# Optimization experiments

Hardware: AMD Instinct MI355X
Metric: run time of the kernel (lower is better)

The kernel has to match this reference:

```python
import jax, jax.numpy as jnp
import numpy as np
from jax import lax

BS, CI, NI, HI, WI = 16, 32, 8, 20, 20
CO, NO = 32, 8
ITERATIONS = 3


def setup_inputs() -> dict:
    key = jax.random.key(0)
    k1, k2 = jax.random.split(key)
    x = jax.random.normal(k1, (BS, CI, NI, HI, WI), dtype=jnp.float32)
    # conv weight: out_channels = co*no = 256, in_channels = ni = 8, 3x3
    W = jax.random.normal(k2, (CO * NO, NI, 3, 3), dtype=jnp.float32) * 0.05
    bias = jnp.zeros((CO, NO, 1, 1), dtype=jnp.float32)
    return {"x": x, "W": W, "bias": bias}


def squash(s, axis):
    # v = (|s|^2 / (1+|s|^2)) * s / |s|
    n2 = jnp.sum(s * s, axis=axis, keepdims=True)
    return s * (n2 / ((1.0 + n2) * jnp.sqrt(n2 + 1e-9)))


def reference(x, W, bias):
    bs, ci, ni, hi, wi = x.shape
    xr = x.reshape(bs * ci, ni, hi, wi)
    # conv2d, stride 1, padding 1, no bias
    votes = lax.conv_general_dilated(
        xr, W, window_strides=(1, 1), padding=[(1, 1), (1, 1)],
        dimension_numbers=("NCHW", "OIHW", "NCHW"))
    ho, wo = votes.shape[-2:]
    votes = votes.reshape(bs, ci, CO, NO, ho, wo)  # (bs,ci,co,no,ho,wo)
    logits = jnp.zeros((bs, ci, CO, ho, wo), dtype=votes.dtype)
    activation = None
    for _ in range(ITERATIONS):
        route = jax.nn.softmax(logits, axis=2)               # (bs,ci,co,ho,wo)
        # weighted sum of votes over input capsules ci, plus bias
        preact = jnp.sum(route[:, :, :, None] * votes, axis=1) + bias  # (bs,co,no,ho,wo)
        activation = squash(preact, axis=2)
        # agreement: dot over output atoms no
        distances = jnp.sum(votes * activation[:, None], axis=3)  # (bs,ci,co,ho,wo)
        logits = logits + distances
    return activation
```

## Files before the change

### kernel.cpp

```cpp
#include <hip/hip_runtime.h>

#define HH 20
#define WW 20

typedef _Float16 f16x8 __attribute__((ext_vector_type(8)));
typedef float    f32x4  __attribute__((ext_vector_type(4)));
typedef float    f32x4u __attribute__((ext_vector_type(4), aligned(4)));

__global__ void prepack_w_kernel(const float* __restrict__ Wt, _Float16* __restrict__ bp) {
    int idx = blockIdx.x * 256 + threadIdx.x;
    int oc = idx / 96, k = idx % 96;
    int r = k >> 3, ni = k & 7;
    float v = (r < 9) ? Wt[oc * 72 + ni * 9 + r] : 0.f;
    bp[idx] = (_Float16)v;
}

template<int DS>
__device__ __forceinline__ void stage_seg(const float* __restrict__ x,
                                          _Float16* A,
                                          int b, int h, int w0, int t) {
#pragma unroll
    for (int s = t; s < 768; s += 256) {
        int ci = s / 24;
        int r  = s % 24;
        int ni = r / 3, hr = r % 3;
        int hh = h - 1 + hr;
        bool hok = (hh >= 0) && (hh < HH);
        const int wlo = (DS == 0) ? (w0 - 1) : (DS < 0 ? 0 : WW - 4);
        const float* rowp = x + ((((b * 32 + ci) * 8 + ni) * HH + (hok ? hh : 0)) * WW) + wlo;
        f32x4u f4 = *(const f32x4u*)rowp;
        float vals[4];
        if (DS == 0)      { vals[0] = f4.x; vals[1] = f4.y; vals[2] = f4.z; vals[3] = f4.w; }
        else if (DS < 0)  { vals[0] = 0.f;  vals[1] = f4.x; vals[2] = f4.y; vals[3] = f4.z; }
        else              { vals[0] = f4.y; vals[1] = f4.z; vals[2] = f4.w; vals[3] = 0.f; }
        int kb = hr * 24 + ni;
#pragma unroll
        for (int j = 0; j < 4; ++j) {
            float v = hok ? vals[j] : 0.f;
            _Float16 hv = (_Float16)v;
            if (j < 3)
                A[ci * 96 + kb + j * 8] = hv;
            if (j > 0)
                A[(32 + ci) * 96 + kb + (j - 1) * 8] = hv;
        }
    }
}

__global__ __launch_bounds__(256, 3)
void caps_mfma8_kernel(const float* __restrict__ x,
                       const _Float16* __restrict__ bp,
                       const float* __restrict__ bias,
                       float* __restrict__ out) {
    __shared__ __align__(16) unsigned char region[30976];
    _Float16* A    = (_Float16*)region;
    float* bufbase = (float*)(region + 12288);

    const int t  = threadIdx.x;
    const int wv = t >> 6;
    const int lr = t & 15;
    const int lg = (t >> 4) & 3;

    const int bi  = blockIdx.x;
    const int b   = bi / 200;
    const int rem = bi % 200;
    const int h   = rem / 10;
    const int w0  = (rem % 10) * 2;

#pragma unroll
    for (int e = t; e < 768; e += 256) {
        int row = e / 12, j = e % 12;
        ((unsigned int*)(A + row * 96 + 72))[j] = 0u;
    }

    const int dshift = (w0 == 0) ? -1 : (w0 == WW - 2) ? 1 : 0;
    if (dshift == 0)      stage_seg<0>(x, A, b, h, w0, t);
    else if (dshift < 0)  stage_seg<-1>(x, A, b, h, w0, t);
    else                  stage_seg<1>(x, A, b, h, w0, t);
    __syncthreads();

    f32x4 acc[4][4];
#pragma unroll
    for (int i = 0; i < 4; ++i)
#pragma unroll
        for (int mt = 0; mt < 4; ++mt) acc[i][mt] = (f32x4){0.f, 0.f, 0.f, 0.f};

#pragma unroll
    for (int mh = 0; mh < 2; ++mh) {
#pragma unroll
        for (int kst = 0; kst < 3; ++kst) {
            const int kb = kst * 32 + lg * 8;
            f16x8 a0 = *(const f16x8*)&A[(mh * 32 + lr) * 96 + kb];
            f16x8 a1 = *(const f16x8*)&A[(mh * 32 + 16 + lr) * 96 + kb];
#pragma unroll
            for (int i = 0; i < 4; ++i) {
                const int oc = (wv * 4 + i) * 16 + lr;
                f16x8 bv = *(const f16x8*)&bp[oc * 96 + kb];
                acc[i][mh*2+0] = __builtin_amdgcn_mfma_f32_16x16x32_f16(a0, bv, acc[i][mh*2+0], 0, 0, 0);
                acc[i][mh*2+1] = __builtin_amdgcn_mfma_f32_16x16x32_f16(a1, bv, acc[i][mh*2+1], 0, 0, 0);
            }
        }
    }

    float* buf = bufbase + wv * 1152;
    float vcol[2][32];
    f32x4 vr[2][4][2];
    const int ch_t = (t >> 5) & 1;
    const int colr = t & 31;
    const int c8   = t & 24;

#pragma unroll
    for (int p = 0; p < 2; ++p) {
#pragma unroll
        for (int ch = 0; ch < 2; ++ch) {
#pragma unroll
            for (int ii = 0; ii < 2; ++ii) {
#pragma unroll
                for (int mm = 0; mm < 2; ++mm) {
#pragma unroll
                    for (int r = 0; r < 4; ++r)
                        buf[(mm * 16 + lg * 4 + r) * 36 + ii * 16 + lr] =
                            acc[ch * 2 + ii][p * 2 + mm][r];
                }
            }
            if (ch_t == ch) {
#pragma unroll
                for (int ci = 0; ci < 32; ++ci) vcol[p][ci] = buf[ci * 36 + colr];
#pragma unroll
                for (int q = 0; q < 4; ++q) {
                    int ciq = (t & 7) * 4 + q;
                    vr[p][q][0] = *(const f32x4*)&buf[ciq * 36 + c8];
                    vr[p][q][1] = *(const f32x4*)&buf[ciq * 36 + c8 + 4];
                }
            }
        }
    }

    const int co = t >> 3;
    const int no = t & 7;
    const float bsv = bias[t];
    float* route0 = bufbase;
    float* route1 = bufbase + 1152;
    float (*lg0)[37] = (float (*)[37])(bufbase + 2304);
    float (*lg1)[37] = (float (*)[37])(bufbase + 2304 + 1184);
    float dlog[2][4];
    float act[2];
    const int lbase = t & 56;

#pragma unroll
    for (int px = 0; px < 2; ++px) {
        float p = 0.f;
#pragma unroll
        for (int ci = 0; ci < 32; ++ci) p += vcol[px][ci];
        p = fmaf(p, 0.03125f, bsv);
        float n2 = p * p;
        n2 += __shfl_xor(n2, 1); n2 += __shfl_xor(n2, 2); n2 += __shfl_xor(n2, 4);
        act[px] = p * n2 * __builtin_amdgcn_rcpf(1.f + n2) * __builtin_amdgcn_rsqf(n2 + 1e-9f);

        float a[8];
#pragma unroll
        for (int j = 0; j < 8; ++j) a[j] = __shfl(act[px], lbase | j);
#pragma unroll
        for (int q = 0; q < 4; ++q) {
            f32x4 v0 = vr[px][q][0], v1 = vr[px][q][1];
            dlog[px][q] = v0.x * a[0] + v0.y * a[1] + v0.z * a[2] + v0.w * a[3]
                        + v1.x * a[4] + v1.y * a[5] + v1.z * a[6] + v1.w * a[7];
        }
    }
    __syncthreads();
#pragma unroll
    for (int px = 0; px < 2; ++px) {
        float (*lgp)[37] = px ? lg1 : lg0;
#pragma unroll
        for (int q = 0; q < 4; ++q) lgp[no * 4 + q][co] = dlog[px][q];
    }
    __syncthreads();

#pragma unroll
    for (int it = 1; it < 3; ++it) {
#pragma unroll
        for (int px = 0; px < 2; ++px) {
            float (*lgp)[37] = px ? lg1 : lg0;
            float* rtp = px ? route1 : route0;
            float l0 = lgp[co][no],      l1 = lgp[co][no + 8];
            float l2 = lgp[co][no + 16], l3 = lgp[co][no + 24];
            float m = fmaxf(fmaxf(l0, l1), fmaxf(l2, l3));
            m = fmaxf(m, __shfl_xor(m, 1)); m = fmaxf(m, __shfl_xor(m, 2)); m = fmaxf(m, __shfl_xor(m, 4));
            float e0 = __expf(l0 - m), e1 = __expf(l1 - m);
            float e2 = __expf(l2 - m), e3 = __expf(l3 - m);
            float s = e0 + e1 + e2 + e3;
            s += __shfl_xor(s, 1); s += __shfl_xor(s, 2); s += __shfl_xor(s, 4);
            float inv = __builtin_amdgcn_rcpf(s);
            rtp[(no)      * 36 + co] = e0 * inv;
            rtp[(no + 8)  * 36 + co] = e1 * inv;
            rtp[(no + 16) * 36 + co] = e2 * inv;
            rtp[(no + 24) * 36 + co] = e3 * inv;
        }
        __syncthreads();

#pragma unroll
        for (int px = 0; px < 2; ++px) {
            float* rtp = px ? route1 : route0;
            float p = bsv;
#pragma unroll
            for (int j = 0; j < 8; ++j) {
                f32x4 rv = *(const f32x4*)&rtp[co * 36 + j * 4];
                p = fmaf(rv.x, vcol[px][j * 4 + 0], p);
                p = fmaf(rv.y, vcol[px][j * 4 + 1], p);
                p = fmaf(rv.z, vcol[px][j * 4 + 2], p);
                p = fmaf(rv.w, vcol[px][j * 4 + 3], p);
            }
            float n2 = p * p;
            n2 += __shfl_xor(n2, 1); n2 += __shfl_xor(n2, 2); n2 += __shfl_xor(n2, 4);
            act[px] = p * n2 * __builtin_amdgcn_rcpf(1.f + n2) * __builtin_amdgcn_rsqf(n2 + 1e-9f);

            if (it == 1) {
                float a[8];
#pragma unroll
                for (int j = 0; j < 8; ++j) a[j] = __shfl(act[px], lbase | j);
                float (*lgp)[37] = px ? lg1 : lg0;
#pragma unroll
                for (int q = 0; q < 4; ++q) {
                    f32x4 v0 = vr[px][q][0], v1 = vr[px][q][1];
                    float d = v0.x * a[0] + v0.y * a[1] + v0.z * a[2] + v0.w * a[3]
                            + v1.x * a[4] + v1.y * a[5] + v1.z * a[6] + v1.w * a[7];
                    dlog[px][q] += d;
                    lgp[no * 4 + q][co] = dlog[px][q];
                }
            }
        }
        if (it == 1) __syncthreads();
    }

    float2 o2 = make_float2(act[0], act[1]);
    *(float2*)&out[(b * 256 + t) * 400 + h * 20 + w0] = o2;
}

extern "C" void kernel_launch(void* const* d_in, const int* in_sizes, int n_in,
                              void* d_out, int out_size, void* d_ws, size_t ws_size,
                              hipStream_t stream) {
    const float* x    = (const float*)d_in[0];
    const float* Wt   = (const float*)d_in[1];
    const float* bias = (const float*)d_in[2];
    float* out        = (float*)d_out;
    _Float16* bp      = (_Float16*)d_ws;

    prepack_w_kernel<<<dim3(96), dim3(256), 0, stream>>>(Wt, bp);
    caps_mfma8_kernel<<<dim3(3200), dim3(256), 0, stream>>>(x, bp, bias, out);
}
```

Before: 59.72 us.

## Drop per-thread vote column, reduce over input capsules with butterfly shuffles

Removes the 64-register vcol array that held each thread's full column of votes across input capsules. The preactivation sum is now computed from the already-held vr fragments and combined across 8 lanes with a butterfly shuffle reduction. Launch bounds rise from 3 to 4 blocks per SM to use the lower register pressure, and the MFMA loop is reordered to load all four A fragments per k-step. The cost is extra cross-lane shuffles in every routing iteration.

```diff
diff --git a/kernel.cpp b/kernel.cpp
--- a/kernel.cpp
+++ b/kernel.cpp
@@ -38,16 +38,29 @@
         for (int j = 0; j < 4; ++j) {
             float v = hok ? vals[j] : 0.f;
             _Float16 hv = (_Float16)v;
-            if (j < 3)
-                A[ci * 96 + kb + j * 8] = hv;
-            if (j > 0)
-                A[(32 + ci) * 96 + kb + (j - 1) * 8] = hv;
-        }
-    }
-}
-
-__global__ __launch_bounds__(256, 3)
-void caps_mfma8_kernel(const float* __restrict__ x,
+            if (j < 3)  A[ci * 96 + kb + j * 8] = hv;
+            if (j > 0)  A[(32 + ci) * 96 + kb + (j - 1) * 8] = hv;
+        }
+    }
+}
+
+__device__ __forceinline__ float bfly8(const float v[8], int lane) {
+    const bool b0 = lane & 1, b1 = lane & 2, b2 = lane & 4;
+    float k0 = b0 ? v[1] : v[0], s0 = b0 ? v[0] : v[1];
+    float k1 = b0 ? v[3] : v[2], s1 = b0 ? v[2] : v[3];
+    float k2 = b0 ? v[5] : v[4], s2 = b0 ? v[4] : v[5];
+    float k3 = b0 ? v[7] : v[6], s3 = b0 ? v[6] : v[7];
+    k0 += __shfl_xor(s0, 1); k1 += __shfl_xor(s1, 1);
+    k2 += __shfl_xor(s2, 1); k3 += __shfl_xor(s3, 1);
+    float m0 = b1 ? k1 : k0, t0 = b1 ? k0 : k1;
+    float m1 = b1 ? k3 : k2, t1 = b1 ? k2 : k3;
+    m0 += __shfl_xor(t0, 2); m1 += __shfl_xor(t1, 2);
+    float r0 = b2 ? m1 : m0, r1 = b2 ? m0 : m1;
+    return r0 + __shfl_xor(r1, 4);
+}
+
+__global__ __launch_bounds__(256, 4)
+void caps_mfma9_kernel(const float* __restrict__ x,
                        const _Float16* __restrict__ bp,
                        const float* __restrict__ bias,
                        float* __restrict__ out) {
@@ -85,27 +98,26 @@
         for (int mt = 0; mt < 4; ++mt) acc[i][mt] = (f32x4){0.f, 0.f, 0.f, 0.f};
 
 #pragma unroll
-    for (int mh = 0; mh < 2; ++mh) {
-#pragma unroll
-        for (int kst = 0; kst < 3; ++kst) {
-            const int kb = kst * 32 + lg * 8;
-            f16x8 a0 = *(const f16x8*)&A[(mh * 32 + lr) * 96 + kb];
-            f16x8 a1 = *(const f16x8*)&A[(mh * 32 + 16 + lr) * 96 + kb];
-#pragma unroll
-            for (int i = 0; i < 4; ++i) {
-                const int oc = (wv * 4 + i) * 16 + lr;
-                f16x8 bv = *(const f16x8*)&bp[oc * 96 + kb];
-                acc[i][mh*2+0] = __builtin_amdgcn_mfma_f32_16x16x32_f16(a0, bv, acc[i][mh*2+0], 0, 0, 0);
-                acc[i][mh*2+1] = __builtin_amdgcn_mfma_f32_16x16x32_f16(a1, bv, acc[i][mh*2+1], 0, 0, 0);
-            }
+    for (int kst = 0; kst < 3; ++kst) {
+        const int kb = kst * 32 + lg * 8;
+        f16x8 af0 = *(const f16x8*)&A[(lr)      * 96 + kb];
+        f16x8 af1 = *(const f16x8*)&A[(16 + lr) * 96 + kb];
+        f16x8 af2 = *(const f16x8*)&A[(32 + lr) * 96 + kb];
+        f16x8 af3 = *(const f16x8*)&A[(48 + lr) * 96 + kb];
+#pragma unroll
+        for (int i = 0; i < 4; ++i) {
+            const int oc = (wv * 4 + i) * 16 + lr;
+            f16x8 bv = *(const f16x8*)&bp[oc * 96 + kb];
+            acc[i][0] = __builtin_amdgcn_mfma_f32_16x16x32_f16(af0, bv, acc[i][0], 0, 0, 0);
+            acc[i][1] = __builtin_amdgcn_mfma_f32_16x16x32_f16(af1, bv, acc[i][1], 0, 0, 0);
+            acc[i][2] = __builtin_amdgcn_mfma_f32_16x16x32_f16(af2, bv, acc[i][2], 0, 0, 0);
+            acc[i][3] = __builtin_amdgcn_mfma_f32_16x16x32_f16(af3, bv, acc[i][3], 0, 0, 0);
         }
     }
 
     float* buf = bufbase + wv * 1152;
-    float vcol[2][32];
     f32x4 vr[2][4][2];
     const int ch_t = (t >> 5) & 1;
-    const int colr = t & 31;
     const int c8   = t & 24;
 
 #pragma unroll
@@ -123,8 +135,6 @@
                 }
             }
             if (ch_t == ch) {
-#pragma unroll
-                for (int ci = 0; ci < 32; ++ci) vcol[p][ci] = buf[ci * 36 + colr];
 #pragma unroll
                 for (int q = 0; q < 4; ++q) {
                     int ciq = (t & 7) * 4 + q;
@@ -148,10 +158,13 @@
 
 #pragma unroll
     for (int px = 0; px < 2; ++px) {
-        float p = 0.f;
-#pragma unroll
-        for (int ci = 0; ci < 32; ++ci) p += vcol[px][ci];
-        p = fmaf(p, 0.03125f, bsv);
+        float pj[8];
+#pragma unroll
+        for (int j = 0; j < 4; ++j) {
+            pj[j]     = vr[px][0][0][j] + vr[px][1][0][j] + vr[px][2][0][j] + vr[px][3][0][j];
+            pj[4 + j] = vr[px][0][1][j] + vr[px][1][1][j] + vr[px][2][1][j] + vr[px][3][1][j];
+        }
+        float p = fmaf(bfly8(pj, t), 0.03125f, bsv);
         float n2 = p * p;
         n2 += __shfl_xor(n2, 1); n2 += __shfl_xor(n2, 2); n2 += __shfl_xor(n2, 4);
         act[px] = p * n2 * __builtin_amdgcn_rcpf(1.f + n2) * __builtin_amdgcn_rsqf(n2 + 1e-9f);
@@ -200,15 +213,16 @@
 #pragma unroll
         for (int px = 0; px < 2; ++px) {
             float* rtp = px ? route1 : route0;
-            float p = bsv;
-#pragma unroll
-            for (int j = 0; j < 8; ++j) {
-                f32x4 rv = *(const f32x4*)&rtp[co * 36 + j * 4];
-                p = fmaf(rv.x, vcol[px][j * 4 + 0], p);
-                p = fmaf(rv.y, vcol[px][j * 4 + 1], p);
-                p = fmaf(rv.z, vcol[px][j * 4 + 2], p);
-                p = fmaf(rv.w, vcol[px][j * 4 + 3], p);
-            }
+            f32x4 rv = *(const f32x4*)&rtp[co * 36 + (t & 7) * 4];
+            float pj[8];
+#pragma unroll
+            for (int j = 0; j < 4; ++j) {
+                pj[j]     = rv.x * vr[px][0][0][j] + rv.y * vr[px][1][0][j]
+                          + rv.z * vr[px][2][0][j] + rv.w * vr[px][3][0][j];
+                pj[4 + j] = rv.x * vr[px][0][1][j] + rv.y * vr[px][1][1][j]
+                          + rv.z * vr[px][2][1][j] + rv.w * vr[px][3][1][j];
+            }
+            float p = bsv + bfly8(pj, t);
             float n2 = p * p;
             n2 += __shfl_xor(n2, 1); n2 += __shfl_xor(n2, 2); n2 += __shfl_xor(n2, 4);
             act[px] = p * n2 * __builtin_amdgcn_rcpf(1.f + n2) * __builtin_amdgcn_rsqf(n2 + 1e-9f);
@@ -245,5 +259,5 @@
     _Float16* bp      = (_Float16*)d_ws;
 
     prepack_w_kernel<<<dim3(96), dim3(256), 0, stream>>>(Wt, bp);
-    caps_mfma8_kernel<<<dim3(3200), dim3(256), 0, stream>>>(x, bp, bias, out);
-}
+    caps_mfma9_kernel<<<dim3(3200), dim3(256), 0, stream>>>(x, bp, bias, out);
+}
```

Result: faster. 54.85 us (-8.2%).
